# Kernel optimization log

Measured on AMD Instinct MI355X. Metric: run time of the kernel, lower is better.

The kernel has to match this reference:

```python
import jax, jax.numpy as jnp
import numpy as np

B, V, K, C = 32, 65536, 8, 3


def setup_inputs() -> dict:
    key = jax.random.key(0)
    k1, k2, k3, k4 = jax.random.split(key, 4)
    out = jax.random.normal(k1, (B, V, C), dtype=jnp.float32)
    tgt = jax.random.normal(k2, (B, V, C), dtype=jnp.float32)
    neighbor_idxs = jax.random.randint(k3, (V, K), 0, V, dtype=jnp.int32)
    # Laplacian weights: each row sums to -1 (lap = x - weighted mean of neighbors)
    w = jax.random.uniform(k4, (V, K), dtype=jnp.float32) + 1e-3
    neighbor_weights = -w / jnp.sum(w, axis=-1, keepdims=True)
    return {
        "out": out,
        "tgt": tgt,
        "neighbor_idxs": neighbor_idxs,
        "neighbor_weights": neighbor_weights,
    }


def _compute_laplacian(x, neighbor_idxs, neighbor_weights):
    # x: [B, V, C]; gather -> [B, V, K, C]; weighted sum over K; residual add
    gathered = x[:, neighbor_idxs]                       # [B, V, K, C]
    return x + jnp.sum(gathered * neighbor_weights[None, :, :, None], axis=2)


def reference(out, tgt, neighbor_idxs, neighbor_weights):
    lap_out = _compute_laplacian(out, neighbor_idxs, neighbor_weights)
    lap_tgt = _compute_laplacian(tgt, neighbor_idxs, neighbor_weights)
    return (lap_out - lap_tgt) ** 2
```

## Files before the change

kernel.cpp:

```cpp
#include <hip/hip_runtime.h>

#define BB 32
#define VV 65536
#define KK 8
#define CC 3

constexpr int NCHUNK = 8;
constexpr int CB     = BB / NCHUNK;
constexpr int CROW   = CB * CC;
constexpr int CROWU  = CROW / 2;

constexpr int TV1   = 64;
constexpr int ROW   = BB * CC;
constexpr int PROW1 = ROW + 1;
constexpr int T1ELEMS = TV1 * ROW;

constexpr int TV2   = 128;
constexpr int PROW2 = CROW + 1;

__device__ __forceinline__ unsigned int f2bf(float f) {
  unsigned int u = __float_as_uint(f);
  u += 0x7FFFu + ((u >> 16) & 1u);
  return u >> 16;
}
__device__ __forceinline__ float bflo(unsigned int u) { return __uint_as_float(u << 16); }
__device__ __forceinline__ float bfhi(unsigned int u) { return __uint_as_float(u & 0xFFFF0000u); }

struct U3 { unsigned int x, y, z; };

__global__ __launch_bounds__(256) void lap_pass1_transpose_sub(
    const float* __restrict__ outp, const float* __restrict__ tgtp,
    unsigned int* __restrict__ dt) {
  __shared__ float tile[TV1 * PROW1];
  const int t  = threadIdx.x;
  const int v0 = blockIdx.x * TV1;

  const float4* o4 = (const float4*)outp;
  const float4* t4 = (const float4*)tgtp;
  const int src_base4 = (v0 * CC) >> 2;
  #pragma unroll
  for (int l4 = t; l4 < T1ELEMS / 4; l4 += 256) {
    int b  = l4 / (TV1 * CC / 4);
    int j4 = l4 - b * (TV1 * CC / 4);
    int src = b * (VV * CC / 4) + src_base4 + j4;
    float4 a = o4[src];
    float4 g = t4[src];
    float dv[4] = {a.x - g.x, a.y - g.y, a.z - g.z, a.w - g.w};
    int j = 4 * j4;
    #pragma unroll
    for (int q = 0; q < 4; q++) {
      int jj = j + q;
      int vrel = jj / CC, c = jj - vrel * CC;
      tile[vrel * PROW1 + b * CC + c] = dv[q];
    }
  }
  __syncthreads();

  #pragma unroll
  for (int u = t; u < NCHUNK * (TV1 * CROWU / 4); u += 256) {
    int chunk = u / (TV1 * CROWU / 4);
    int i16   = u - chunk * (TV1 * CROWU / 4);
    int E = i16 * 8;
    unsigned int w[8];
    #pragma unroll
    for (int q = 0; q < 8; q++) {
      int ee = E + q;
      int vrel = ee / CROW, jj = ee - vrel * CROW;
      w[q] = f2bf(tile[vrel * PROW1 + chunk * CROW + jj]);
    }
    uint4 o;
    o.x = w[0] | (w[1] << 16);
    o.y = w[2] | (w[3] << 16);
    o.z = w[4] | (w[5] << 16);
    o.w = w[6] | (w[7] << 16);
    uint4* dst = (uint4*)(dt + (size_t)chunk * (VV * CROWU) + (size_t)v0 * CROWU);
    dst[i16] = o;
  }
}

__global__ __launch_bounds__(256) void lap_pass2_gather(
    const unsigned int* __restrict__ dt, const int* __restrict__ nidx,
    const float* __restrict__ nw, float* __restrict__ res) {
  __shared__ float rtile[TV2 * PROW2];
  __shared__ int   idx_s[TV2 * KK];
  __shared__ float w_s[TV2 * KK];
  const int t     = threadIdx.x;
  const int chunk = blockIdx.x & (NCHUNK - 1);
  const int v0    = (blockIdx.x >> 3) * TV2;

  ((int4*)idx_s)[t]  = ((const int4*)(nidx + (size_t)v0 * KK))[t];
  ((float4*)w_s)[t]  = ((const float4*)(nw + (size_t)v0 * KK))[t];
  __syncthreads();

  const unsigned int* dtc = dt + (size_t)chunk * (VV * CROWU);
  const int vrel = t >> 1;
  const int l    = t & 1;
  const int v    = v0 + vrel;

  const int4*   ip = (const int4*)&idx_s[vrel * KK];
  const float4* wp = (const float4*)&w_s[vrel * KK];
  int4   ia = ip[0], ib = ip[1];
  float4 wa = wp[0], wb = wp[1];
  int   nbk[KK] = {ia.x, ia.y, ia.z, ia.w, ib.x, ib.y, ib.z, ib.w};
  float wk[KK]  = {wa.x, wa.y, wa.z, wa.w, wb.x, wb.y, wb.z, wb.w};

  U3 s = *(const U3*)(dtc + (size_t)v * CROWU + 3 * l);
  float x0 = bflo(s.x), y0 = bfhi(s.x), z0 = bflo(s.y);
  float x1 = bfhi(s.y), y1 = bflo(s.z), z1 = bfhi(s.z);

  #pragma unroll
  for (int k = 0; k < KK; k++) {
    U3 u = *(const U3*)(dtc + (size_t)nbk[k] * CROWU + 3 * l);
    const float wt = wk[k];
    x0 = fmaf(wt, bflo(u.x), x0);
    y0 = fmaf(wt, bfhi(u.x), y0);
    z0 = fmaf(wt, bflo(u.y), z0);
    x1 = fmaf(wt, bfhi(u.y), x1);
    y1 = fmaf(wt, bflo(u.z), y1);
    z1 = fmaf(wt, bfhi(u.z), z1);
  }
  float* rp = &rtile[vrel * PROW2 + 6 * l];
  rp[0] = x0 * x0; rp[1] = y0 * y0; rp[2] = z0 * z0;
  rp[3] = x1 * x1; rp[4] = y1 * y1; rp[5] = z1 * z1;
  __syncthreads();

  float4* r4 = (float4*)res;
  const int dst_base4 = (v0 * CC) >> 2;
  #pragma unroll
  for (int l4 = t; l4 < CB * (TV2 * CC / 4); l4 += 256) {
    int b  = l4 / (TV2 * CC / 4);
    int j4 = l4 - b * (TV2 * CC / 4);
    int bg = chunk * CB + b;
    int j  = 4 * j4;
    float tmp[4];
    #pragma unroll
    for (int q = 0; q < 4; q++) {
      int jj = j + q;
      int vr = jj / CC, c = jj - vr * CC;
      tmp[q] = rtile[vr * PROW2 + b * CC + c];
    }
    r4[bg * (VV * CC / 4) + dst_base4 + j4] = make_float4(tmp[0], tmp[1], tmp[2], tmp[3]);
  }
}

__global__ __launch_bounds__(256) void lap_fused_fallback(
    const float* __restrict__ outp, const float* __restrict__ tgtp,
    const int* __restrict__ nidx, const float* __restrict__ nw,
    float* __restrict__ res) {
  int tid = blockIdx.x * 256 + threadIdx.x;
  if (tid >= BB * VV) return;
  int v = tid & (VV - 1);
  int b = tid >> 16;
  float ax = 0.f, ay = 0.f, az = 0.f;
  #pragma unroll
  for (int k = 0; k < KK; k++) {
    int   nb = nidx[v * KK + k];
    float wt = nw[v * KK + k];
    const float* po = outp + ((size_t)b * VV + nb) * CC;
    const float* pt = tgtp + ((size_t)b * VV + nb) * CC;
    ax = fmaf(wt, po[0] - pt[0], ax);
    ay = fmaf(wt, po[1] - pt[1], ay);
    az = fmaf(wt, po[2] - pt[2], az);
  }
  const float* so = outp + (size_t)tid * CC;
  const float* st = tgtp + (size_t)tid * CC;
  float dx = so[0] - st[0] + ax;
  float dy = so[1] - st[1] + ay;
  float dz = so[2] - st[2] + az;
  float* rp = res + (size_t)tid * CC;
  rp[0] = dx * dx; rp[1] = dy * dy; rp[2] = dz * dz;
}

extern "C" void kernel_launch(void* const* d_in, const int* in_sizes, int n_in,
                              void* d_out, int out_size, void* d_ws, size_t ws_size,
                              hipStream_t stream) {
  const float* outp = (const float*)d_in[0];
  const float* tgtp = (const float*)d_in[1];
  const int*   nidx = (const int*)d_in[2];
  const float* nw   = (const float*)d_in[3];
  float* res = (float*)d_out;

  const size_t dt_bytes = (size_t)VV * ROW * 2;
  if (ws_size >= dt_bytes) {
    unsigned int* dt = (unsigned int*)d_ws;
    lap_pass1_transpose_sub<<<VV / TV1, 256, 0, stream>>>(outp, tgtp, dt);
    lap_pass2_gather<<<NCHUNK * (VV / TV2), 256, 0, stream>>>(dt, nidx, nw, res);
  } else {
    lap_fused_fallback<<<(BB * VV) / 256, 256, 0, stream>>>(outp, tgtp, nidx, nw, res);
  }
}
```

Measured before the change: 120.9 us.

## Use persistent XCD-affine work-stealing gather with four batch chunks

The gather pass becomes a persistent kernel. Each block reads its XCD id from a hardware register and claims vertex tiles from the chunk counter tied to that XCD, stealing from other chunks once its own runs out. Because each chunk's bf16 slice is then read mostly by a single XCD, the aim is to keep neighbour gathers in that XCD's L2 instead of every XCD pulling every chunk. The chunk count falls to four, so each slice holds eight batches, and the tile shrinks to 64 vertices. The cost is atomic counter traffic, extra barriers per tile, and reliance on how XCD ids map to chunks.

```diff
diff --git a/kernel.cpp b/kernel.cpp
--- a/kernel.cpp
+++ b/kernel.cpp
@@ -5,7 +5,7 @@
 #define KK 8
 #define CC 3
 
-constexpr int NCHUNK = 8;
+constexpr int NCHUNK = 4;
 constexpr int CB     = BB / NCHUNK;
 constexpr int CROW   = CB * CC;
 constexpr int CROWU  = CROW / 2;
@@ -15,8 +15,10 @@
 constexpr int PROW1 = ROW + 1;
 constexpr int T1ELEMS = TV1 * ROW;
 
-constexpr int TV2   = 128;
-constexpr int PROW2 = CROW + 1;
+constexpr int TVG   = 64;
+constexpr int PR2   = CROW + 1;
+constexpr int NTILE = VV / TVG;
+constexpr int G2    = 4096;
 
 __device__ __forceinline__ unsigned int f2bf(float f) {
   unsigned int u = __float_as_uint(f);
@@ -30,10 +32,12 @@
 
 __global__ __launch_bounds__(256) void lap_pass1_transpose_sub(
     const float* __restrict__ outp, const float* __restrict__ tgtp,
-    unsigned int* __restrict__ dt) {
+    unsigned int* __restrict__ dt, unsigned int* __restrict__ ctr) {
   __shared__ float tile[TV1 * PROW1];
   const int t  = threadIdx.x;
   const int v0 = blockIdx.x * TV1;
+
+  if (blockIdx.x == 0 && t < NCHUNK) atomicExch(&ctr[t], 0u);
 
   const float4* o4 = (const float4*)outp;
   const float4* t4 = (const float4*)tgtp;
@@ -80,66 +84,88 @@
 
 __global__ __launch_bounds__(256) void lap_pass2_gather(
     const unsigned int* __restrict__ dt, const int* __restrict__ nidx,
-    const float* __restrict__ nw, float* __restrict__ res) {
-  __shared__ float rtile[TV2 * PROW2];
-  __shared__ int   idx_s[TV2 * KK];
-  __shared__ float w_s[TV2 * KK];
-  const int t     = threadIdx.x;
-  const int chunk = blockIdx.x & (NCHUNK - 1);
-  const int v0    = (blockIdx.x >> 3) * TV2;
-
-  ((int4*)idx_s)[t]  = ((const int4*)(nidx + (size_t)v0 * KK))[t];
-  ((float4*)w_s)[t]  = ((const float4*)(nw + (size_t)v0 * KK))[t];
-  __syncthreads();
-
-  const unsigned int* dtc = dt + (size_t)chunk * (VV * CROWU);
-  const int vrel = t >> 1;
-  const int l    = t & 1;
-  const int v    = v0 + vrel;
-
-  const int4*   ip = (const int4*)&idx_s[vrel * KK];
-  const float4* wp = (const float4*)&w_s[vrel * KK];
-  int4   ia = ip[0], ib = ip[1];
-  float4 wa = wp[0], wb = wp[1];
-  int   nbk[KK] = {ia.x, ia.y, ia.z, ia.w, ib.x, ib.y, ib.z, ib.w};
-  float wk[KK]  = {wa.x, wa.y, wa.z, wa.w, wb.x, wb.y, wb.z, wb.w};
-
-  U3 s = *(const U3*)(dtc + (size_t)v * CROWU + 3 * l);
-  float x0 = bflo(s.x), y0 = bfhi(s.x), z0 = bflo(s.y);
-  float x1 = bfhi(s.y), y1 = bflo(s.z), z1 = bfhi(s.z);
-
-  #pragma unroll
-  for (int k = 0; k < KK; k++) {
-    U3 u = *(const U3*)(dtc + (size_t)nbk[k] * CROWU + 3 * l);
-    const float wt = wk[k];
-    x0 = fmaf(wt, bflo(u.x), x0);
-    y0 = fmaf(wt, bfhi(u.x), y0);
-    z0 = fmaf(wt, bflo(u.y), z0);
-    x1 = fmaf(wt, bfhi(u.y), x1);
-    y1 = fmaf(wt, bflo(u.z), y1);
-    z1 = fmaf(wt, bfhi(u.z), z1);
-  }
-  float* rp = &rtile[vrel * PROW2 + 6 * l];
-  rp[0] = x0 * x0; rp[1] = y0 * y0; rp[2] = z0 * z0;
-  rp[3] = x1 * x1; rp[4] = y1 * y1; rp[5] = z1 * z1;
-  __syncthreads();
-
-  float4* r4 = (float4*)res;
-  const int dst_base4 = (v0 * CC) >> 2;
-  #pragma unroll
-  for (int l4 = t; l4 < CB * (TV2 * CC / 4); l4 += 256) {
-    int b  = l4 / (TV2 * CC / 4);
-    int j4 = l4 - b * (TV2 * CC / 4);
-    int bg = chunk * CB + b;
-    int j  = 4 * j4;
-    float tmp[4];
-    #pragma unroll
-    for (int q = 0; q < 4; q++) {
-      int jj = j + q;
-      int vr = jj / CC, c = jj - vr * CC;
-      tmp[q] = rtile[vr * PROW2 + b * CC + c];
-    }
-    r4[bg * (VV * CC / 4) + dst_base4 + j4] = make_float4(tmp[0], tmp[1], tmp[2], tmp[3]);
+    const float* __restrict__ nw, float* __restrict__ res,
+    unsigned int* __restrict__ ctr) {
+  __shared__ float rtile[TVG * PR2];
+  __shared__ int   idx_s[TVG * KK];
+  __shared__ float w_s[TVG * KK];
+  __shared__ int   s_claim[2];
+  const int t = threadIdx.x;
+
+  const int xcd = __builtin_amdgcn_s_getreg((3 << 11) | 20);
+  const int myq = xcd & (NCHUNK - 1);
+
+  for (;;) {
+    if (t == 0) {
+      int got = -1, gq = -1;
+      #pragma unroll
+      for (int a = 0; a < NCHUNK; a++) {
+        int qq = (myq + a) & (NCHUNK - 1);
+        unsigned int s = atomicAdd(&ctr[qq], 1u);
+        if (s < (unsigned int)NTILE) { got = (int)s; gq = qq; break; }
+      }
+      s_claim[0] = got; s_claim[1] = gq;
+    }
+    __syncthreads();
+    const int tilei = s_claim[0], q = s_claim[1];
+    if (tilei < 0) break;
+    const int v0 = tilei * TVG;
+
+    ((int2*)idx_s)[t]  = ((const int2*)(nidx + (size_t)v0 * KK))[t];
+    ((float2*)w_s)[t]  = ((const float2*)(nw + (size_t)v0 * KK))[t];
+    __syncthreads();
+
+    const unsigned int* dtc = dt + (size_t)q * (VV * CROWU);
+    const int gr = t >> 2;
+    const int la = t & 3;
+    const int v  = v0 + gr;
+
+    const int4*   ip = (const int4*)&idx_s[gr * KK];
+    const float4* wp = (const float4*)&w_s[gr * KK];
+    int4   ia = ip[0], ib = ip[1];
+    float4 wa = wp[0], wb = wp[1];
+    int   nbk[KK] = {ia.x, ia.y, ia.z, ia.w, ib.x, ib.y, ib.z, ib.w};
+    float wk[KK]  = {wa.x, wa.y, wa.z, wa.w, wb.x, wb.y, wb.z, wb.w};
+
+    U3 s = *(const U3*)(dtc + (size_t)v * CROWU + 3 * la);
+    float x0 = bflo(s.x), y0 = bfhi(s.x), z0 = bflo(s.y);
+    float x1 = bfhi(s.y), y1 = bflo(s.z), z1 = bfhi(s.z);
+
+    #pragma unroll
+    for (int k = 0; k < KK; k++) {
+      U3 u = *(const U3*)(dtc + (size_t)nbk[k] * CROWU + 3 * la);
+      const float wt = wk[k];
+      x0 = fmaf(wt, bflo(u.x), x0);
+      y0 = fmaf(wt, bfhi(u.x), y0);
+      z0 = fmaf(wt, bflo(u.y), z0);
+      x1 = fmaf(wt, bfhi(u.y), x1);
+      y1 = fmaf(wt, bflo(u.z), y1);
+      z1 = fmaf(wt, bfhi(u.z), z1);
+    }
+    float* rp = &rtile[gr * PR2 + 6 * la];
+    rp[0] = x0 * x0; rp[1] = y0 * y0; rp[2] = z0 * z0;
+    rp[3] = x1 * x1; rp[4] = y1 * y1; rp[5] = z1 * z1;
+    __syncthreads();
+
+    float4* r4 = (float4*)res;
+    const int dst_base4 = (v0 * CC) >> 2;
+    #pragma unroll
+    for (int l4 = t; l4 < CB * (TVG * CC / 4); l4 += 256) {
+      int bb = l4 / (TVG * CC / 4);
+      int j4 = l4 - bb * (TVG * CC / 4);
+      int b  = q * CB + bb;
+      int j  = 4 * j4;
+      float tmp[4];
+      #pragma unroll
+      for (int e = 0; e < 4; e++) {
+        int jj = j + e;
+        int vr = jj / CC, c = jj - vr * CC;
+        tmp[e] = rtile[vr * PR2 + bb * CC + c];
+      }
+      r4[(size_t)b * (VV * CC / 4) + dst_base4 + j4] =
+          make_float4(tmp[0], tmp[1], tmp[2], tmp[3]);
+    }
+    __syncthreads();
   }
 }
 
@@ -181,10 +207,11 @@
   float* res = (float*)d_out;
 
   const size_t dt_bytes = (size_t)VV * ROW * 2;
-  if (ws_size >= dt_bytes) {
-    unsigned int* dt = (unsigned int*)d_ws;
-    lap_pass1_transpose_sub<<<VV / TV1, 256, 0, stream>>>(outp, tgtp, dt);
-    lap_pass2_gather<<<NCHUNK * (VV / TV2), 256, 0, stream>>>(dt, nidx, nw, res);
+  if (ws_size >= dt_bytes + 4 * sizeof(unsigned int)) {
+    unsigned int* dt  = (unsigned int*)d_ws;
+    unsigned int* ctr = dt + (size_t)VV * CROWU * NCHUNK;
+    lap_pass1_transpose_sub<<<VV / TV1, 256, 0, stream>>>(outp, tgtp, dt, ctr);
+    lap_pass2_gather<<<G2, 256, 0, stream>>>(dt, nidx, nw, res, ctr);
   } else {
     lap_fused_fallback<<<(BB * VV) / 256, 256, 0, stream>>>(outp, tgtp, nidx, nw, res);
   }
```

Result: slower. 330.9 us (+173.7%).
